# Kernel optimization log

Hardware: AMD Instinct MI355X
Metric: run time of the kernel (lower is better)

The kernel has to match this reference:

```python
import jax, jax.numpy as jnp
import numpy as np
from functools import partial

TAU = 2.0
BN_EPS = 1e-5
SG_ALPHA = 4.0  # spikingjelly surrogate.Sigmoid default

@jax.custom_vjp
def heaviside(x):
    return (x >= 0.0).astype(x.dtype)

def _heaviside_fwd(x):
    return heaviside(x), x

def _heaviside_bwd(x, g):
    s = jax.nn.sigmoid(SG_ALPHA * x)
    return (g * SG_ALPHA * s * (1.0 - s),)

heaviside.defvjp(_heaviside_fwd, _heaviside_bwd)

def lif(x_seq, v_threshold=1.0):
    # MultiStepLIFNode: tau=2, decay_input=True, v_reset=0 (hard reset), detach_reset
    def step(v, x):
        v = v + (x - v) / TAU
        s = heaviside(v - v_threshold)
        v = v * (1.0 - jax.lax.stop_gradient(s))
        return v, s
    _, s_seq = jax.lax.scan(step, jnp.zeros_like(x_seq[0]), x_seq)
    return s_seq

def conv1x1_bn(x, w, gamma, beta, mean, var, b=None):
    # x: [T,B,C,N]; w: [Cout,Cin]; 1x1 conv == channel matmul; BN in eval mode
    y = jnp.einsum('oc,tbcn->tbon', w, x)
    if b is not None:
        y = y + b[:, None]
    inv = gamma / jnp.sqrt(var + BN_EPS)
    return y * inv[:, None] + (beta - mean * inv)[:, None]

def setup_inputs() -> dict:
    key = jax.random.key(0)
    ks = jax.random.split(key, 24)
    T, B, C, N = 4, 32, 384, 196
    d = {}
    d['x'] = jax.random.normal(ks[0], (T, B, C, N), dtype=jnp.float32)
    d['policy'] = jax.random.uniform(ks[1], (T * B, N, 1), dtype=jnp.float32)
    scale = 1.0 / np.sqrt(C)
    for i, p in enumerate(['q', 'k', 'v', 'proj']):
        base = 2 + i * 5
        d[p + '_w'] = jax.random.normal(ks[base], (C, C), dtype=jnp.float32) * scale
        d[p + '_gamma'] = jnp.ones((C,), jnp.float32)
        d[p + '_beta'] = jnp.zeros((C,), jnp.float32)
        d[p + '_mean'] = jax.random.normal(ks[base + 1], (C,), dtype=jnp.float32) * 0.1
        d[p + '_var'] = jax.random.uniform(ks[base + 2], (C,), dtype=jnp.float32, minval=0.5, maxval=1.5)
    d['proj_b'] = jnp.zeros((C,), jnp.float32)
    return d

def _to_heads(s, H):
    T, B, C, N = s.shape
    # [T,B,C,N] -> [T,B,N,H,D] -> [T,B,H,N,D]
    return s.transpose(0, 1, 3, 2).reshape(T, B, N, H, C // H).transpose(0, 1, 3, 2, 4)

def reference(x, policy, q_w, q_gamma, q_beta, q_mean, q_var,
              k_w, k_gamma, k_beta, k_mean, k_var,
              v_w, v_gamma, v_beta, v_mean, v_var,
              proj_w, proj_gamma, proj_beta, proj_mean, proj_var, proj_b):
    T, B, C, N = x.shape
    H = 12
    attn_scale = 0.25
    q = _to_heads(lif(conv1x1_bn(x, q_w, q_gamma, q_beta, q_mean, q_var)), H)
    k = _to_heads(lif(conv1x1_bn(x, k_w, k_gamma, k_beta, k_mean, k_var)), H)
    v = _to_heads(lif(conv1x1_bn(x, v_w, v_gamma, v_beta, v_mean, v_var)), H)
    attn = jnp.einsum('tbhnd,tbhmd->tbhnm', q, k)
    # attention_policy: attn *= (policy + (1-policy)*eye)
    pol = policy.reshape(T, B, 1, 1, N)
    eye = jnp.eye(N, dtype=attn.dtype)
    attn = attn * (pol + (1.0 - pol) * eye)
    y = jnp.einsum('tbhnm,tbhmd->tbhnd', attn, v) * attn_scale
    y = y.transpose(0, 1, 2, 4, 3).reshape(T, B, C, N)
    y = lif(y, v_threshold=0.5)
    y = conv1x1_bn(y, proj_w, proj_gamma, proj_beta, proj_mean, proj_var, b=proj_b)
    return lif(y)
```

## Files before the change

kernel.cpp:

```cpp
#include <hip/hip_runtime.h>

typedef unsigned int u32;
typedef __bf16 bf16x8 __attribute__((ext_vector_type(8)));
typedef __bf16 bf16x4v __attribute__((ext_vector_type(4)));
typedef _Float16 f16x8 __attribute__((ext_vector_type(8)));
typedef float f32x4 __attribute__((ext_vector_type(4)));

#define Tn 4
#define Bn 32
#define Cn 384
#define Nn 196
#define Hn 12
#define CNn (Cn*Nn)
#define BCNn (Bn*CNn)
#define BHNn (Bn*Hn*Nn)
#define PBITS (Tn*BHNn)
#define TBCNn (Tn*BCNn)
#define NCOLS 6272
#define WSZ 147456

__device__ __forceinline__ void split3(float v, __bf16& h, __bf16& m, __bf16& l) {
  h = (__bf16)v;  float r = v - (float)h;
  m = (__bf16)r;  float r2 = r - (float)m;
  l = (__bf16)r2;
}
__device__ __forceinline__ void split2h(float v, _Float16& h, _Float16& l) {
  h = (_Float16)v;  l = (_Float16)(v - (float)h);
}

__device__ __forceinline__ void gl_lds16(const void* g, void* l) {
  __builtin_amdgcn_global_load_lds(
      (const __attribute__((address_space(1))) unsigned int*)g,
      (__attribute__((address_space(3))) unsigned int*)l, 16, 0, 0);
}

struct WSplitArgs {
  const float* w[4]; const float* g[4]; const float* be[4];
  const float* mu[4]; const float* va[4]; const float* bias;
};
__global__ __launch_bounds__(256) void split_w(
    WSplitArgs a, _Float16* __restrict__ wsp16, __bf16* __restrict__ wspb,
    float* __restrict__ shv) {
  const int i = blockIdx.x * 256 + threadIdx.x;
  const int p = i / WSZ, r = i - p * WSZ;
  const int o = r / Cn;
  const float iv = a.g[p][o] / sqrtf(a.va[p][o] + 1e-5f);
  const float wv = a.w[p][r] * iv;
  if (p < 3) {
    _Float16 h, l;
    split2h(wv, h, l);
    wsp16[(size_t)(p * 2 + 0) * WSZ + r] = h;
    wsp16[(size_t)(p * 2 + 1) * WSZ + r] = l;
  } else {
    __bf16 h, m, l;
    split3(wv, h, m, l);
    wspb[(size_t)0 * WSZ + r] = h;
    wspb[(size_t)1 * WSZ + r] = m;
    wspb[(size_t)2 * WSZ + r] = l;
  }
  if (r - o * Cn == 0) {
    float sh = a.be[p][o] - a.mu[p][o] * iv;
    if (p == 3) sh += a.bias[o] * iv;
    shv[p * Cn + o] = sh;
  }
}

__global__ __launch_bounds__(256) void transpose_split_x(
    const float* __restrict__ x, _Float16* __restrict__ xs) {
  __shared__ float tile[49 * 130];
  const int t = blockIdx.x, b = blockIdx.y;
  const int ct = blockIdx.z >> 2, nch = blockIdx.z & 3;
  const int c0 = ct * 128, n0 = nch * 49;
  const int tid = threadIdx.x;
  for (int idx = tid; idx < 49 * 128; idx += 256) {
    const int n = idx % 49, c = idx / 49;
    tile[n * 130 + c] = x[(size_t)t * BCNn + (size_t)b * CNn +
                          (size_t)(c0 + c) * Nn + n0 + n];
  }
  __syncthreads();
  for (int idx = tid; idx < 49 * 64; idx += 256) {
    const int cp = idx & 63, n = idx >> 6;
    const float v0 = tile[n * 130 + cp * 2];
    const float v1 = tile[n * 130 + cp * 2 + 1];
    _Float16 h0, l0, h1, l1;
    split2h(v0, h0, l0);
    split2h(v1, h1, l1);
    const size_t col = (size_t)t * NCOLS + (size_t)b * Nn + n0 + n;
    union { _Float16 f[2]; u32 u; } uh, ul;
    uh.f[0] = h0; uh.f[1] = h1;
    ul.f[0] = l0; ul.f[1] = l1;
    ((u32*)(xs + col * Cn + c0))[cp] = uh.u;
    ((u32*)(xs + (size_t)TBCNn + col * Cn + c0))[cp] = ul.u;
  }
}

__global__ __launch_bounds__(256, 2) void gemm_qkv_lif(
    const _Float16* __restrict__ xs,
    const _Float16* __restrict__ wsp16,
    const float* __restrict__ shv,
    u32* __restrict__ bq, u32* __restrict__ bk, u32* __restrict__ bv)
{
  __shared__ _Float16 Asw[3][2][128][32];
  __shared__ _Float16 Bsw[3][2][64][32];
  const int orig = blockIdx.x;
  const int xcd = orig & 7, i8 = orig >> 3;
  const int wgid = xcd * 110 + (xcd < 2 ? xcd : 2) + i8;
  const int colt = wgid / 9, v = wgid - colt * 9;
  const int col0 = colt * 64;
  const int p = v / 3, mt = v - p * 3;
  const int o0 = mt * 128;
  const int tid = threadIdx.x, lane = tid & 63, wid = tid >> 6;
  const int wm = wid >> 1, wn = wid & 1;
  const int quad = lane >> 4, nl = lane & 15;
  u32* __restrict__ bits = (p == 0) ? bq : (p == 1) ? bk : bv;

  u32 aOff[4], bOff[2];
#pragma unroll
  for (int i = 0; i < 4; ++i) {
    const int c = i * 256 + wid * 64 + lane;
    const int s = c >> 9, row = (c >> 2) & 127, kb = c & 3;
    const int kbs = kb ^ ((row >> 1) & 3);
    aOff[i] = (u32)((((p * 2 + s) * WSZ) + (o0 + row) * Cn + kbs * 8) * 2);
  }
#pragma unroll
  for (int i = 0; i < 2; ++i) {
    const int c = i * 256 + wid * 64 + lane;
    const int s = c >> 8, rem = c & 255, row = rem >> 2, kb = rem & 3;
    const int kbs = kb ^ ((row >> 1) & 3);
    bOff[i] = (u32)(((size_t)s * TBCNn + (size_t)(col0 + row) * Cn + kbs * 8) * 2);
  }
  const char* wB = (const char*)wsp16;
  const char* xB = (const char*)xs;
  char* aD0 = (char*)&Asw[0][0][0][0] + wid * 1024;
  char* bD0 = (char*)&Bsw[0][0][0][0] + wid * 1024;

#define STAGE_A(ai_) do {                                                  \
    const u32 ak_ = (u32)(((ai_) % 12) * 64);                              \
    char* d_ = aD0 + ((ai_) % 3) * 16384;                                  \
    _Pragma("unroll") for (int i_ = 0; i_ < 4; ++i_)                       \
      gl_lds16(wB + aOff[i_] + ak_, d_ + i_ * 4096);                       \
  } while (0)
#define STAGE_B(g_) do {                                                   \
    const int t_ = ((g_) / 24) * 2 + ((g_) & 1);                           \
    const int kk_ = (((g_) % 24) >> 1);                                    \
    const u32 bk_ = (u32)(kk_ * 64) + (u32)t_ * (u32)(NCOLS * Cn * 2);     \
    char* d_ = bD0 + ((g_) % 3) * 8192;                                    \
    _Pragma("unroll") for (int i_ = 0; i_ < 2; ++i_)                       \
      gl_lds16(xB + bOff[i_] + bk_, d_ + i_ * 4096);                       \
  } while (0)

  f32x4 sh_[4];
#pragma unroll
  for (int mi = 0; mi < 4; ++mi)
    sh_[mi] = *(const f32x4*)&shv[p * Cn + o0 + wm * 64 + mi * 16 + quad * 4];

  f32x4 acc0[4][2], acc1[4][2];
  f32x4 vst[4][2] = {};

  auto epi = [&](f32x4 (&ac)[4][2], int t) {
#pragma unroll
    for (int ni = 0; ni < 2; ++ni) {
      u32 w0 = 0, w1 = 0;
#pragma unroll
      for (int mi = 0; mi < 4; ++mi) {
#pragma unroll
        for (int r = 0; r < 4; ++r) {
          const float y = ac[mi][ni][r] + sh_[mi][r];
          const float vv = vst[mi][ni][r];
          const float nv = vv + (y - vv) * 0.5f;
          const bool sk = nv >= 1.0f;
          vst[mi][ni][r] = sk ? 0.f : nv;
          const u32 b1 = sk ? 1u : 0u;
          const int pos = ((mi & 1) << 4) + (quad << 2) + r;
          if (mi < 2) w0 |= b1 << pos; else w1 |= b1 << pos;
        }
      }
      w0 |= __shfl_xor(w0, 16); w0 |= __shfl_xor(w0, 32);
      w1 |= __shfl_xor(w1, 16); w1 |= __shfl_xor(w1, 32);
      if (quad == 0) {
        const int col = col0 + wn * 32 + ni * 16 + nl;
        const int bb = col / Nn, nn = col - bb * Nn;
        u32* bp = bits + (size_t)t * BHNn +
                  ((size_t)bb * Hn + (mt * 4 + wm * 2)) * Nn + nn;
        bp[0] = w0;
        bp[Nn] = w1;
      }
    }
  };

  STAGE_B(0); STAGE_A(0); STAGE_B(1); STAGE_A(1);

#pragma unroll 1
  for (int gg = 0; gg < 24; ++gg) {
    const int abuf = gg % 3;
    const int be = (2 * gg) % 3, bo = (2 * gg + 1) % 3;
    const int kk = gg % 12;

    if (gg < 23) { asm volatile("s_waitcnt vmcnt(6)" ::: "memory"); }
    else         { asm volatile("s_waitcnt vmcnt(2)" ::: "memory"); }
    __builtin_amdgcn_s_barrier();
    __builtin_amdgcn_sched_barrier(0);
    if (gg < 23) STAGE_B(2 * gg + 2);
    if (kk == 0) {
#pragma unroll
      for (int mi = 0; mi < 4; ++mi)
#pragma unroll
        for (int ni = 0; ni < 2; ++ni) {
          acc0[mi][ni] = f32x4{0.f, 0.f, 0.f, 0.f};
          acc1[mi][ni] = f32x4{0.f, 0.f, 0.f, 0.f};
        }
    }
    f16x8 af0[4], af1[4];
#pragma unroll
    for (int mi = 0; mi < 4; ++mi) {
      const int ra = wm * 64 + mi * 16 + nl;
      const int ka = (quad ^ ((ra >> 1) & 3)) * 8;
      af0[mi] = *(const f16x8*)&Asw[abuf][0][ra][ka];
      af1[mi] = *(const f16x8*)&Asw[abuf][1][ra][ka];
    }
    {
      f16x8 bfr[2][2];
#pragma unroll
      for (int i = 0; i < 2; ++i) {
        const int rb = wn * 32 + i * 16 + nl;
        const int kb2 = (quad ^ ((rb >> 1) & 3)) * 8;
        bfr[0][i] = *(const f16x8*)&Bsw[be][0][rb][kb2];
        bfr[1][i] = *(const f16x8*)&Bsw[be][1][rb][kb2];
      }
      __builtin_amdgcn_s_setprio(1);
#pragma unroll
      for (int mi = 0; mi < 4; ++mi)
#pragma unroll
        for (int ni = 0; ni < 2; ++ni) {
          f32x4 c = acc0[mi][ni];
          c = __builtin_amdgcn_mfma_f32_16x16x32_f16(af0[mi], bfr[0][ni], c, 0, 0, 0);
          c = __builtin_amdgcn_mfma_f32_16x16x32_f16(af0[mi], bfr[1][ni], c, 0, 0, 0);
          c = __builtin_amdgcn_mfma_f32_16x16x32_f16(af1[mi], bfr[0][ni], c, 0, 0, 0);
          acc0[mi][ni] = c;
        }
      __builtin_amdgcn_s_setprio(0);
    }

    if (gg < 23) { asm volatile("s_waitcnt vmcnt(6)" ::: "memory"); }
    else         { asm volatile("s_waitcnt vmcnt(0)" ::: "memory"); }
    __builtin_amdgcn_s_barrier();
    __builtin_amdgcn_sched_barrier(0);
    if (gg < 23) STAGE_B(2 * gg + 3);
    if (gg < 22) STAGE_A(gg + 2);
    {
      f16x8 bfr[2][2];
#pragma unroll
      for (int i = 0; i < 2; ++i) {
        const int rb = wn * 32 + i * 16 + nl;
        const int kb2 = (quad ^ ((rb >> 1) & 3)) * 8;
        bfr[0][i] = *(const f16x8*)&Bsw[bo][0][rb][kb2];
        bfr[1][i] = *(const f16x8*)&Bsw[bo][1][rb][kb2];
      }
      __builtin_amdgcn_s_setprio(1);
#pragma unroll
      for (int mi = 0; mi < 4; ++mi)
#pragma unroll
        for (int ni = 0; ni < 2; ++ni) {
          f32x4 c = acc1[mi][ni];
          c = __builtin_amdgcn_mfma_f32_16x16x32_f16(af0[mi], bfr[0][ni], c, 0, 0, 0);
          c = __builtin_amdgcn_mfma_f32_16x16x32_f16(af0[mi], bfr[1][ni], c, 0, 0, 0);
          c = __builtin_amdgcn_mfma_f32_16x16x32_f16(af1[mi], bfr[0][ni], c, 0, 0, 0);
          acc1[mi][ni] = c;
        }
      __builtin_amdgcn_s_setprio(0);
    }
    if (kk == 11) {
      const int p2 = gg / 12;
      epi(acc0, p2 * 2 + 0);
      epi(acc1, p2 * 2 + 1);
    }
  }
#undef STAGE_A
#undef STAGE_B
}

#define ASTR 40
__global__ __launch_bounds__(256) void attn_lif(
    const u32* __restrict__ qb, const u32* __restrict__ kb,
    const u32* __restrict__ vb, const float* __restrict__ policy,
    __bf16* __restrict__ sp) {
  __shared__ u32 qs[208], ks[224], vs_[224];
  __shared__ float ps[224];
  __shared__ __bf16 psp[3][224];
  __shared__ __bf16 Al[208 * ASTR];
  __shared__ __bf16 Ul[3][32 * ASTR];
  const int bh = blockIdx.x;
  const int bN = bh / Hn;
  const int h = bh - bN * Hn;
  const int tid = threadIdx.x;
  const int lane = tid & 63, wid = tid >> 6;
  const int quad = lane >> 4, nl = lane & 15;

  float vst[4][2][4] = {};

  for (int t = 0; t < Tn; ++t) {
    const int tb = t * Bn + bN;
    const int gid = tb * Hn + h;
    if (t) __syncthreads();
    for (int i = tid; i < 224; i += 256) {
      const bool in = i < Nn;
      if (i < 208) qs[i] = in ? qb[(size_t)gid * Nn + i] : 0u;
      ks[i] = in ? kb[(size_t)gid * Nn + i] : 0u;
      vs_[i] = in ? vb[(size_t)gid * Nn + i] : 0u;
      const float p = in ? policy[(size_t)tb * Nn + i] : 0.f;
      ps[i] = p;
      __bf16 hh, mm, ll;
      split3(p, hh, mm, ll);
      psp[0][i] = hh; psp[1][i] = mm; psp[2][i] = ll;
    }
    __syncthreads();

    f32x4 acc[4][2] = {};

    for (int slab = 0; slab < 7; ++slab) {
      const int m0 = slab * 32;
      if (tid < 208) {
        const u32 qn = qs[tid];
        __bf16 a32[32];
#pragma unroll
        for (int mk = 0; mk < 32; ++mk)
          a32[mk] = (__bf16)(float)__popc(qn & ks[m0 + mk]);
#pragma unroll
        for (int g = 0; g < 4; ++g)
          *(bf16x8*)&Al[tid * ASTR + g * 8] = *(bf16x8*)&a32[g * 8];
      }
      {
        const int dp = tid >> 3, mkg = (tid & 7) * 4;
        __bf16 u4[3][4];
#pragma unroll
        for (int j = 0; j < 4; ++j) {
          const int m = m0 + mkg + j;
          const bool bit = (vs_[m] >> dp) & 1u;
#pragma unroll
          for (int s = 0; s < 3; ++s)
            u4[s][j] = bit ? psp[s][m] : (__bf16)0.f;
        }
#pragma unroll
        for (int s = 0; s < 3; ++s)
          *(bf16x4v*)&Ul[s][dp * ASTR + mkg] = *(bf16x4v*)u4[s];
      }
      __syncthreads();
      bf16x8 bfr[3][2];
#pragma unroll
      for (int s = 0; s < 3; ++s)
#pragma unroll
        for (int nt = 0; nt < 2; ++nt)
          bfr[s][nt] = *(const bf16x8*)&Ul[s][(nt * 16 + nl) * ASTR + quad * 8];
#pragma unroll
      for (int mi = 0; mi < 4; ++mi) {
        const int mt2 = wid + mi * 4;
        if (mt2 < 13) {
          const bf16x8 af = *(const bf16x8*)&Al[(mt2 * 16 + nl) * ASTR + quad * 8];
#pragma unroll
          for (int nt = 0; nt < 2; ++nt) {
            f32x4 c = acc[mi][nt];
            c = __builtin_amdgcn_mfma_f32_16x16x32_bf16(af, bfr[0][nt], c, 0, 0, 0);
            c = __builtin_amdgcn_mfma_f32_16x16x32_bf16(af, bfr[1][nt], c, 0, 0, 0);
            c = __builtin_amdgcn_mfma_f32_16x16x32_bf16(af, bfr[2][nt], c, 0, 0, 0);
            acc[mi][nt] = c;
          }
        }
      }
      __syncthreads();
    }
#pragma unroll
    for (int mi = 0; mi < 4; ++mi) {
      const int mt2 = wid + mi * 4;
      if (mt2 >= 13) continue;
#pragma unroll
      for (int r = 0; r < 4; ++r) {
        const int n = mt2 * 16 + quad * 4 + r;
        if (n >= Nn) continue;
        const float ann = (float)__popc(qs[n] & ks[n]);
        const float wd = ann * (1.0f - ps[n]);
        const u32 vn = vs_[n];
        __bf16* op = sp + (size_t)t * BCNn + ((size_t)bN * Nn + n) * Cn + h * 32;
#pragma unroll
        for (int nt = 0; nt < 2; ++nt) {
          const int d = nt * 16 + nl;
          const float bit = (float)((vn >> d) & 1u);
          const float y = (acc[mi][nt][r] + wd * bit) * 0.25f;
          const float vv = vst[mi][nt][r];
          const float nv = vv + (y - vv) * 0.5f;
          const bool s = nv >= 0.5f;
          vst[mi][nt][r] = s ? 0.f : nv;
          op[d] = (__bf16)(s ? 1.0f : 0.0f);
        }
      }
    }
  }
}

__global__ __launch_bounds__(256, 3) void gemm_proj_mfma(
    const __bf16* __restrict__ sp, const __bf16* __restrict__ wspb,
    const float* __restrict__ shv, float* __restrict__ z)
{
  __shared__ __bf16 Asw[3][128][32];
  __shared__ __bf16 Bsw[128][32];
  const int bid = blockIdx.x;
  const int xcd = bid & 7, slot = bid >> 3;
  const int gl = slot / 3, mt = slot - gl * 3;
  const int group = xcd * 25 + gl;
  if (group >= 196) return;
  const int colt = group % 49, t = group / 49;
  const int col0 = colt * 128, o0 = mt * 128;
  const int tid = threadIdx.x, lane = tid & 63, wid = tid >> 6;
  const int wm = wid >> 1, wn = wid & 1;
  const int quad = lane >> 4, nl = lane & 15;
  const __bf16* Bg = sp + ((size_t)t * NCOLS + col0) * Cn;

  f32x4 acc[4][4] = {};
  bf16x8 aval[6], bval[2];
#pragma unroll
  for (int i = 0; i < 6; ++i) {
    const int u = tid + i * 256, s = u >> 9, rem = u & 511;
    const int row = rem >> 2, kb = rem & 3;
    aval[i] = *(const bf16x8*)(wspb + (size_t)s * WSZ + (size_t)(o0 + row) * Cn + kb * 8);
  }
#pragma unroll
  for (int i = 0; i < 2; ++i) {
    const int u = tid + i * 256, row = u >> 2, kb = u & 3;
    bval[i] = *(const bf16x8*)(Bg + (size_t)row * Cn + kb * 8);
  }

  for (int kk = 0; kk < 12; ++kk) {
    __syncthreads();
#pragma unroll
    for (int i = 0; i < 6; ++i) {
      const int u = tid + i * 256, s = u >> 9, rem = u & 511;
      const int row = rem >> 2, kb = rem & 3;
      const int kbp = kb ^ ((row >> 1) & 3);
      *(bf16x8*)&Asw[s][row][kbp * 8] = aval[i];
    }
#pragma unroll
    for (int i = 0; i < 2; ++i) {
      const int u = tid + i * 256, row = u >> 2, kb = u & 3;
      const int kbp = kb ^ ((row >> 1) & 3);
      *(bf16x8*)&Bsw[row][kbp * 8] = bval[i];
    }
    __syncthreads();
    if (kk < 11) {
      const int k0n = (kk + 1) * 32;
#pragma unroll
      for (int i = 0; i < 6; ++i) {
        const int u = tid + i * 256, s = u >> 9, rem = u & 511;
        const int row = rem >> 2, kb = rem & 3;
        aval[i] = *(const bf16x8*)(wspb + (size_t)s * WSZ +
                                   (size_t)(o0 + row) * Cn + k0n + kb * 8);
      }
#pragma unroll
      for (int i = 0; i < 2; ++i) {
        const int u = tid + i * 256, row = u >> 2, kb = u & 3;
        bval[i] = *(const bf16x8*)(Bg + (size_t)row * Cn + k0n + kb * 8);
      }
    }
    bf16x8 af[3][4], bfr[4];
#pragma unroll
    for (int i = 0; i < 4; ++i) {
      const int ra = wm * 64 + i * 16 + nl;
      const int rb = wn * 64 + i * 16 + nl;
      const int ka = (quad ^ ((ra >> 1) & 3)) * 8;
      const int kb2 = (quad ^ ((rb >> 1) & 3)) * 8;
      bfr[i] = *(const bf16x8*)&Bsw[rb][kb2];
#pragma unroll
      for (int s = 0; s < 3; ++s)
        af[s][i] = *(const bf16x8*)&Asw[s][ra][ka];
    }
#pragma unroll
    for (int mi = 0; mi < 4; ++mi)
#pragma unroll
      for (int ni = 0; ni < 4; ++ni) {
        f32x4 c = acc[mi][ni];
        c = __builtin_amdgcn_mfma_f32_16x16x32_bf16(af[0][mi], bfr[ni], c, 0, 0, 0);
        c = __builtin_amdgcn_mfma_f32_16x16x32_bf16(af[1][mi], bfr[ni], c, 0, 0, 0);
        c = __builtin_amdgcn_mfma_f32_16x16x32_bf16(af[2][mi], bfr[ni], c, 0, 0, 0);
        acc[mi][ni] = c;
      }
  }
#pragma unroll
  for (int mi = 0; mi < 4; ++mi) {
    const int ob = o0 + wm * 64 + mi * 16 + quad * 4;
    const f32x4 sh4 = *(const f32x4*)&shv[3 * Cn + ob];
#pragma unroll
    for (int ni = 0; ni < 4; ++ni) {
      const int col = col0 + wn * 64 + ni * 16 + nl;
      const int b = col / Nn, nn = col - b * Nn;
      float* zp = z + (size_t)t * BCNn + (size_t)b * CNn + nn;
#pragma unroll
      for (int r = 0; r < 4; ++r)
        zp[(size_t)(ob + r) * Nn] = acc[mi][ni][r] + sh4[r];
    }
  }
}

__global__ __launch_bounds__(256) void lif_out_v4(
    const float* __restrict__ z, float* __restrict__ out) {
  const size_t i4 = ((size_t)blockIdx.x * 256 + threadIdx.x) * 4;
  f32x4 v = {0.f, 0.f, 0.f, 0.f};
#pragma unroll
  for (int t = 0; t < Tn; ++t) {
    f32x4 x = *(const f32x4*)(z + (size_t)t * BCNn + i4);
    f32x4 o4;
#pragma unroll
    for (int r = 0; r < 4; ++r) {
      const float nv = v[r] + (x[r] - v[r]) * 0.5f;
      const bool s = nv >= 1.0f;
      o4[r] = s ? 1.0f : 0.0f;
      v[r] = s ? 0.f : nv;
    }
    *(f32x4*)(out + (size_t)t * BCNn + i4) = o4;
  }
}

extern "C" void kernel_launch(void* const* d_in, const int* in_sizes, int n_in,
                              void* d_out, int out_size, void* d_ws, size_t ws_size,
                              hipStream_t stream) {
  const float* x      = (const float*)d_in[0];
  const float* policy = (const float*)d_in[1];
  const float* qw = (const float*)d_in[2];
  const float* qg = (const float*)d_in[3];
  const float* qb_ = (const float*)d_in[4];
  const float* qm = (const float*)d_in[5];
  const float* qv = (const float*)d_in[6];
  const float* kw = (const float*)d_in[7];
  const float* kg = (const float*)d_in[8];
  const float* kbe = (const float*)d_in[9];
  const float* km = (const float*)d_in[10];
  const float* kv = (const float*)d_in[11];
  const float* vw = (const float*)d_in[12];
  const float* vg = (const float*)d_in[13];
  const float* vbe = (const float*)d_in[14];
  const float* vm = (const float*)d_in[15];
  const float* vv = (const float*)d_in[16];
  const float* pw = (const float*)d_in[17];
  const float* pg = (const float*)d_in[18];
  const float* pbe = (const float*)d_in[19];
  const float* pm = (const float*)d_in[20];
  const float* pv = (const float*)d_in[21];
  const float* pbias = (const float*)d_in[22];
  float* out = (float*)d_out;

  char* base = (char*)d_ws;
  _Float16* xs   = (_Float16*)base;
  _Float16* wsp16 = (_Float16*)(base + (size_t)TBCNn * 4);
  __bf16* wspb   = (__bf16*)((char*)wsp16 + (size_t)6 * WSZ * 2);
  float* shv     = (float*)((char*)wspb + (size_t)3 * WSZ * 2);
  u32* bq        = (u32*)((char*)shv + 4 * Cn * 4);
  u32* bk = bq + PBITS;
  u32* bv = bk + PBITS;
  __bf16* sp     = (__bf16*)(bv + PBITS);
  float* z       = (float*)((char*)sp + (size_t)TBCNn * 2);

  WSplitArgs wa;
  wa.w[0] = qw; wa.g[0] = qg; wa.be[0] = qb_; wa.mu[0] = qm; wa.va[0] = qv;
  wa.w[1] = kw; wa.g[1] = kg; wa.be[1] = kbe; wa.mu[1] = km; wa.va[1] = kv;
  wa.w[2] = vw; wa.g[2] = vg; wa.be[2] = vbe; wa.mu[2] = vm; wa.va[2] = vv;
  wa.w[3] = pw; wa.g[3] = pg; wa.be[3] = pbe; wa.mu[3] = pm; wa.va[3] = pv;
  wa.bias = pbias;
  split_w<<<2304, 256, 0, stream>>>(wa, wsp16, wspb, shv);
  transpose_split_x<<<dim3(4, 32, 12), 256, 0, stream>>>(x, xs);

  gemm_qkv_lif<<<882, 256, 0, stream>>>(xs, wsp16, shv, bq, bk, bv);
  attn_lif<<<Bn * Hn, 256, 0, stream>>>(bq, bk, bv, policy, sp);
  gemm_proj_mfma<<<600, 256, 0, stream>>>(sp, wspb, shv, z);
  lif_out_v4<<<BCNn / 1024, 256, 0, stream>>>(z, out);
}
```

Baseline: 307.6 us.

## Fuse prep kernels, split attention rows across two blocks, use direct-to-LDS loads in proj GEMM

Merges the weight-split and x-transpose kernels into one launch, which removes a kernel launch and lets the two jobs overlap. The attention kernel is split so each (batch, head) is handled by two blocks owning 112 and 84 query rows, doubling the grid from 384 blocks and giving the 256 CUs more parallelism. Each half-block recomputes the V/policy staging, which is duplicated work. The projection GEMM replaces register-staged prefetch with global_load_lds direct copies into the swizzled LDS tiles. That removes register staging, but it also drops the overlap of the next tile's loads with the current MFMAs, since loads are now issued and waited on within each k-step.

```diff
diff --git a/kernel.cpp b/kernel.cpp
--- a/kernel.cpp
+++ b/kernel.cpp
@@ -38,40 +38,42 @@
   const float* w[4]; const float* g[4]; const float* be[4];
   const float* mu[4]; const float* va[4]; const float* bias;
 };
-__global__ __launch_bounds__(256) void split_w(
+__global__ __launch_bounds__(256) void prep(
     WSplitArgs a, _Float16* __restrict__ wsp16, __bf16* __restrict__ wspb,
-    float* __restrict__ shv) {
-  const int i = blockIdx.x * 256 + threadIdx.x;
-  const int p = i / WSZ, r = i - p * WSZ;
-  const int o = r / Cn;
-  const float iv = a.g[p][o] / sqrtf(a.va[p][o] + 1e-5f);
-  const float wv = a.w[p][r] * iv;
-  if (p < 3) {
-    _Float16 h, l;
-    split2h(wv, h, l);
-    wsp16[(size_t)(p * 2 + 0) * WSZ + r] = h;
-    wsp16[(size_t)(p * 2 + 1) * WSZ + r] = l;
-  } else {
-    __bf16 h, m, l;
-    split3(wv, h, m, l);
-    wspb[(size_t)0 * WSZ + r] = h;
-    wspb[(size_t)1 * WSZ + r] = m;
-    wspb[(size_t)2 * WSZ + r] = l;
-  }
-  if (r - o * Cn == 0) {
-    float sh = a.be[p][o] - a.mu[p][o] * iv;
-    if (p == 3) sh += a.bias[o] * iv;
-    shv[p * Cn + o] = sh;
-  }
-}
-
-__global__ __launch_bounds__(256) void transpose_split_x(
-    const float* __restrict__ x, _Float16* __restrict__ xs) {
+    float* __restrict__ shv, const float* __restrict__ x,
+    _Float16* __restrict__ xs) {
   __shared__ float tile[49 * 130];
-  const int t = blockIdx.x, b = blockIdx.y;
-  const int ct = blockIdx.z >> 2, nch = blockIdx.z & 3;
+  const int bx = blockIdx.x;
+  const int tid = threadIdx.x;
+  if (bx < 2304) {
+    const int i = bx * 256 + tid;
+    const int p = i / WSZ, r = i - p * WSZ;
+    const int o = r / Cn;
+    const float iv = a.g[p][o] / sqrtf(a.va[p][o] + 1e-5f);
+    const float wv = a.w[p][r] * iv;
+    if (p < 3) {
+      _Float16 h, l;
+      split2h(wv, h, l);
+      wsp16[(size_t)(p * 2 + 0) * WSZ + r] = h;
+      wsp16[(size_t)(p * 2 + 1) * WSZ + r] = l;
+    } else {
+      __bf16 h, m, l;
+      split3(wv, h, m, l);
+      wspb[(size_t)0 * WSZ + r] = h;
+      wspb[(size_t)1 * WSZ + r] = m;
+      wspb[(size_t)2 * WSZ + r] = l;
+    }
+    if (r - o * Cn == 0) {
+      float sh = a.be[p][o] - a.mu[p][o] * iv;
+      if (p == 3) sh += a.bias[o] * iv;
+      shv[p * Cn + o] = sh;
+    }
+    return;
+  }
+  const int bid2 = bx - 2304;
+  const int t = bid2 & 3, b = (bid2 >> 2) & 31, zz = bid2 >> 7;
+  const int ct = zz >> 2, nch = zz & 3;
   const int c0 = ct * 128, n0 = nch * 49;
-  const int tid = threadIdx.x;
   for (int idx = tid; idx < 49 * 128; idx += 256) {
     const int n = idx % 49, c = idx / 49;
     tile[n * 130 + c] = x[(size_t)t * BCNn + (size_t)b * CNn +
@@ -287,16 +289,21 @@
   __shared__ u32 qs[208], ks[224], vs_[224];
   __shared__ float ps[224];
   __shared__ __bf16 psp[3][224];
-  __shared__ __bf16 Al[208 * ASTR];
+  __shared__ __bf16 Al[112 * ASTR];
   __shared__ __bf16 Ul[3][32 * ASTR];
-  const int bh = blockIdx.x;
+  const int blk = blockIdx.x;
+  const int half = blk & 1;
+  const int bh = blk >> 1;
   const int bN = bh / Hn;
   const int h = bh - bN * Hn;
+  const int nbase = half * 112;
+  const int ntiles = half ? 6 : 7;
+  const int nrows = ntiles * 16;
   const int tid = threadIdx.x;
   const int lane = tid & 63, wid = tid >> 6;
   const int quad = lane >> 4, nl = lane & 15;
 
-  float vst[4][2][4] = {};
+  float vst[2][2][4] = {};
 
   for (int t = 0; t < Tn; ++t) {
     const int tb = t * Bn + bN;
@@ -315,12 +322,12 @@
     }
     __syncthreads();
 
-    f32x4 acc[4][2] = {};
+    f32x4 acc[2][2] = {};
 
     for (int slab = 0; slab < 7; ++slab) {
       const int m0 = slab * 32;
-      if (tid < 208) {
-        const u32 qn = qs[tid];
+      if (tid < nrows) {
+        const u32 qn = qs[nbase + tid];
         __bf16 a32[32];
 #pragma unroll
         for (int mk = 0; mk < 32; ++mk)
@@ -352,10 +359,10 @@
         for (int nt = 0; nt < 2; ++nt)
           bfr[s][nt] = *(const bf16x8*)&Ul[s][(nt * 16 + nl) * ASTR + quad * 8];
 #pragma unroll
-      for (int mi = 0; mi < 4; ++mi) {
-        const int mt2 = wid + mi * 4;
-        if (mt2 < 13) {
-          const bf16x8 af = *(const bf16x8*)&Al[(mt2 * 16 + nl) * ASTR + quad * 8];
+      for (int mi = 0; mi < 2; ++mi) {
+        const int lt = wid + mi * 4;
+        if (lt < ntiles) {
+          const bf16x8 af = *(const bf16x8*)&Al[(lt * 16 + nl) * ASTR + quad * 8];
 #pragma unroll
           for (int nt = 0; nt < 2; ++nt) {
             f32x4 c = acc[mi][nt];
@@ -369,12 +376,12 @@
       __syncthreads();
     }
 #pragma unroll
-    for (int mi = 0; mi < 4; ++mi) {
-      const int mt2 = wid + mi * 4;
-      if (mt2 >= 13) continue;
+    for (int mi = 0; mi < 2; ++mi) {
+      const int lt = wid + mi * 4;
+      if (lt >= ntiles) continue;
 #pragma unroll
       for (int r = 0; r < 4; ++r) {
-        const int n = mt2 * 16 + quad * 4 + r;
+        const int n = nbase + lt * 16 + quad * 4 + r;
         if (n >= Nn) continue;
         const float ann = (float)__popc(qs[n] & ks[n]);
         const float wd = ann * (1.0f - ps[n]);
@@ -414,51 +421,36 @@
   const int quad = lane >> 4, nl = lane & 15;
   const __bf16* Bg = sp + ((size_t)t * NCOLS + col0) * Cn;
 
+  const char* aSrc[6];
+  const char* bSrc[2];
+#pragma unroll
+  for (int i = 0; i < 6; ++i) {
+    const int c = i * 256 + wid * 64 + lane;
+    const int s = c >> 9, rem = c & 511;
+    const int row = rem >> 2, kb = rem & 3;
+    const int kbs = kb ^ ((row >> 1) & 3);
+    aSrc[i] = (const char*)(wspb + (size_t)s * WSZ +
+                            (size_t)(o0 + row) * Cn + kbs * 8);
+  }
+#pragma unroll
+  for (int i = 0; i < 2; ++i) {
+    const int c = i * 256 + wid * 64 + lane;
+    const int row = c >> 2, kb = c & 3;
+    const int kbs = kb ^ ((row >> 1) & 3);
+    bSrc[i] = (const char*)(Bg + (size_t)row * Cn + kbs * 8);
+  }
+  char* aDst = (char*)&Asw[0][0][0] + wid * 1024;
+  char* bDst = (char*)&Bsw[0][0] + wid * 1024;
+
   f32x4 acc[4][4] = {};
-  bf16x8 aval[6], bval[2];
-#pragma unroll
-  for (int i = 0; i < 6; ++i) {
-    const int u = tid + i * 256, s = u >> 9, rem = u & 511;
-    const int row = rem >> 2, kb = rem & 3;
-    aval[i] = *(const bf16x8*)(wspb + (size_t)s * WSZ + (size_t)(o0 + row) * Cn + kb * 8);
-  }
-#pragma unroll
-  for (int i = 0; i < 2; ++i) {
-    const int u = tid + i * 256, row = u >> 2, kb = u & 3;
-    bval[i] = *(const bf16x8*)(Bg + (size_t)row * Cn + kb * 8);
-  }
 
   for (int kk = 0; kk < 12; ++kk) {
+    const int koff = kk * 64;
+#pragma unroll
+    for (int i = 0; i < 6; ++i) gl_lds16(aSrc[i] + koff, aDst + i * 4096);
+#pragma unroll
+    for (int i = 0; i < 2; ++i) gl_lds16(bSrc[i] + koff, bDst + i * 4096);
     __syncthreads();
-#pragma unroll
-    for (int i = 0; i < 6; ++i) {
-      const int u = tid + i * 256, s = u >> 9, rem = u & 511;
-      const int row = rem >> 2, kb = rem & 3;
-      const int kbp = kb ^ ((row >> 1) & 3);
-      *(bf16x8*)&Asw[s][row][kbp * 8] = aval[i];
-    }
-#pragma unroll
-    for (int i = 0; i < 2; ++i) {
-      const int u = tid + i * 256, row = u >> 2, kb = u & 3;
-      const int kbp = kb ^ ((row >> 1) & 3);
-      *(bf16x8*)&Bsw[row][kbp * 8] = bval[i];
-    }
-    __syncthreads();
-    if (kk < 11) {
-      const int k0n = (kk + 1) * 32;
-#pragma unroll
-      for (int i = 0; i < 6; ++i) {
-        const int u = tid + i * 256, s = u >> 9, rem = u & 511;
-        const int row = rem >> 2, kb = rem & 3;
-        aval[i] = *(const bf16x8*)(wspb + (size_t)s * WSZ +
-                                   (size_t)(o0 + row) * Cn + k0n + kb * 8);
-      }
-#pragma unroll
-      for (int i = 0; i < 2; ++i) {
-        const int u = tid + i * 256, row = u >> 2, kb = u & 3;
-        bval[i] = *(const bf16x8*)(Bg + (size_t)row * Cn + k0n + kb * 8);
-      }
-    }
     bf16x8 af[3][4], bfr[4];
 #pragma unroll
     for (int i = 0; i < 4; ++i) {
@@ -481,6 +473,7 @@
         c = __builtin_amdgcn_mfma_f32_16x16x32_bf16(af[2][mi], bfr[ni], c, 0, 0, 0);
         acc[mi][ni] = c;
       }
+    __syncthreads();
   }
 #pragma unroll
   for (int mi = 0; mi < 4; ++mi) {
@@ -562,11 +555,10 @@
   wa.w[2] = vw; wa.g[2] = vg; wa.be[2] = vbe; wa.mu[2] = vm; wa.va[2] = vv;
   wa.w[3] = pw; wa.g[3] = pg; wa.be[3] = pbe; wa.mu[3] = pm; wa.va[3] = pv;
   wa.bias = pbias;
-  split_w<<<2304, 256, 0, stream>>>(wa, wsp16, wspb, shv);
-  transpose_split_x<<<dim3(4, 32, 12), 256, 0, stream>>>(x, xs);
+  prep<<<3840, 256, 0, stream>>>(wa, wsp16, wspb, shv, x, xs);
 
   gemm_qkv_lif<<<882, 256, 0, stream>>>(xs, wsp16, shv, bq, bk, bv);
-  attn_lif<<<Bn * Hn, 256, 0, stream>>>(bq, bk, bv, policy, sp);
+  attn_lif<<<2 * Bn * Hn, 256, 0, stream>>>(bq, bk, bv, policy, sp);
   gemm_proj_mfma<<<600, 256, 0, stream>>>(sp, wspb, shv, z);
   lif_out_v4<<<BCNn / 1024, 256, 0, stream>>>(z, out);
 }
```

Measured after the change: 296.9 us. -3.5%, faster.
